# Kernel optimization log

Hardware: AMD Instinct MI355X
Metric: run time of the kernel (lower is better)

The kernel has to match this reference:

```python
import jax, jax.numpy as jnp
import numpy as np

H = 1024          # hidden_size
E = 2 * H         # expansion e
S_DIM = 128       # shared q/k dim s
B, S = 4, 2048


def setup_inputs() -> dict:
    key = jax.random.key(0)
    ks = jax.random.split(key, 6)
    inputs = jax.random.normal(ks[0], (B, S, H), dtype=jnp.float32)
    W_uv = jax.random.normal(ks[1], (H, 2 * E + S_DIM), dtype=jnp.float32) * (1.0 / np.sqrt(H))
    b_uv = jnp.zeros((2 * E + S_DIM,), dtype=jnp.float32)
    gamma = jax.random.normal(ks[2], (2, S_DIM), dtype=jnp.float32) * 0.02
    beta = jnp.zeros((2, S_DIM), dtype=jnp.float32)
    W_out = jax.random.normal(ks[3], (E, H), dtype=jnp.float32) * (1.0 / np.sqrt(E))
    b_out = jnp.zeros((H,), dtype=jnp.float32)
    return {"inputs": inputs, "W_uv": W_uv, "b_uv": b_uv,
            "gamma": gamma, "beta": beta, "W_out": W_out, "b_out": b_out}


def reference(inputs, W_uv, b_uv, gamma, beta, W_out, b_out):
    seq_len = inputs.shape[1]
    # uv projection + SiLU
    uvb = jax.nn.silu(jnp.einsum('bsh,hf->bsf', inputs, W_uv) + b_uv)
    u = uvb[..., :E]                       # [B,S,E]
    v = uvb[..., E:2 * E]                  # [B,S,E]
    base = uvb[..., 2 * E:]                # [B,S,s]
    # per-head affine: [B,S,1,s]*[2,s] + [2,s] -> [B,S,2,s]
    qk = base[..., None, :] * gamma + beta
    q, k = qk[..., 0, :], qk[..., 1, :]    # [B,S,s] each
    scores = jnp.einsum('bns,bms->bnm', q, k) / seq_len   # [B,S,S]
    sq = jnp.square(jax.nn.relu(scores))
    attn_v = jnp.einsum('bnm,bme->bne', sq, v)            # [B,S,E]
    return jnp.einsum('bne,eh->bnh', u * attn_v, W_out) + b_out
```

## Files before the change

### kernel.cpp

```cpp
#include <hip/hip_runtime.h>
#include <stdint.h>


#define H_DIM  1024
#define E_DIM  2048
#define SD     128
#define B_SZ   4
#define S_LEN  2048
#define M_TOT  (B_SZ * S_LEN)
#define F_DIM  (2 * E_DIM + SD)

typedef _Float16 f16;
typedef __attribute__((ext_vector_type(4))) _Float16 f16x4;
typedef __attribute__((ext_vector_type(8))) _Float16 f16x8;
typedef __attribute__((ext_vector_type(16))) float f32x16;

__device__ __forceinline__ float silu_f(float x) { return x / (1.f + __expf(-x)); }

__device__ __forceinline__ void gload16(const void* g, void* l) {
  __builtin_amdgcn_global_load_lds(
      (const __attribute__((address_space(1))) void*)(uintptr_t)g,
      (__attribute__((address_space(3))) void*)(uint32_t)(uintptr_t)l,
      16, 0, 0);
}

__global__ __launch_bounds__(256) void cast_f16_k(const float* __restrict__ src,
                                                  f16* __restrict__ dst, long n) {
  long i = ((long)blockIdx.x * 256 + threadIdx.x) * 4;
  if (i < n) {
    float4 v = *(const float4*)(src + i);
    f16x4 h; h[0] = (f16)v.x; h[1] = (f16)v.y; h[2] = (f16)v.z; h[3] = (f16)v.w;
    *(f16x4*)(dst + i) = h;
  }
}

__global__ __launch_bounds__(256) void transpose_cast_k(const float* __restrict__ src,
                                                        f16* __restrict__ dst, int R, int C) {
  __shared__ float tile[32][33];
  int c0 = blockIdx.x * 32, r0 = blockIdx.y * 32;
  int tx = threadIdx.x & 31, ty = threadIdx.x >> 5;
  for (int i = ty; i < 32; i += 8) tile[i][tx] = src[(long)(r0 + i) * C + c0 + tx];
  __syncthreads();
  for (int i = ty; i < 32; i += 8) dst[(long)(c0 + i) * R + r0 + tx] = (f16)tile[tx][i];
}

template <int MODE>
__global__ __launch_bounds__(512, 2) void gemm256(
    const f16* __restrict__ Ag, const f16* __restrict__ Bg,
    float* __restrict__ F0, f16* __restrict__ O0, f16* __restrict__ O1,
    const f16* __restrict__ I0, const float* __restrict__ C0)
{
  constexpr int K  = (MODE == 0) ? H_DIM : 2048;
  constexpr int NT = K / 64;

  __shared__ f16 As[2][256][64];
  __shared__ f16 Bs[2][256][64];

  const int t    = threadIdx.x;
  const int w    = t >> 6;
  const int lane = t & 63;
  const int lo5  = lane & 31;
  const int hi   = lane >> 5;
  const int wm   = w >> 2;
  const int wn   = w & 3;

  const int gx  = gridDim.x;
  const int nwg = gx * gridDim.y;
  const int lin = blockIdx.y * gx + blockIdx.x;
  const int cpx = nwg >> 3;
  const int wg  = (lin & 7) * cpx + (lin >> 3);
  const int n0  = (wg % gx) * 256;
  const int m0  = (wg / gx) * 256;
  const long z  = blockIdx.z;

  const f16* A = Ag + (MODE == 2 ? z * (long)S_LEN * S_LEN : 0);
  const f16* B = Bg + (MODE == 2 ? z * (long)E_DIM * S_LEN : 0);

  auto stageA = [&](int bb, int half, int kt2) {
    const f16* g0 = A + (long)(m0 + half * 128) * K + kt2 * 64;
    f16* lb = &As[bb][half * 128][0];
#pragma unroll
    for (int j = 0; j < 2; j++) {
      int grp = (j << 3) + w;
      int rl  = (grp << 3) + (lane >> 3);
      gload16(g0 + (long)rl * K + (((lane & 7) ^ (lane >> 3) ^ (grp & 1)) << 3),
              lb + (grp << 9));
    }
  };
  auto stageB = [&](int bb, int half, int kt2) {
    const f16* g0 = B + (long)(n0 + half * 128) * K + kt2 * 64;
    f16* lb = &Bs[bb][half * 128][0];
#pragma unroll
    for (int j = 0; j < 2; j++) {
      int grp = (j << 3) + w;
      int rl  = (grp << 3) + (lane >> 3);
      gload16(g0 + (long)rl * K + (((lane & 7) ^ (lane >> 3) ^ (grp & 1)) << 3),
              lb + (grp << 9));
    }
  };

  f32x16 acc[4][2] = {};
  f16x8 a0[2][4], a1[2][4], b0[4], b1[4];

  const int swz = (lo5 & 7) ^ ((lo5 >> 3) & 1);
  const int rA  = wm * 64 + lo5;
  const int rB  = wn * 32 + lo5;

  auto loadA0 = [&](int bb) {
#pragma unroll
    for (int k = 0; k < 4; k++) {
      const int pc = ((((k << 1) + hi) ^ swz) << 3);
      a0[0][k] = *(const f16x8*)&As[bb][rA][pc];
      a0[1][k] = *(const f16x8*)&As[bb][rA + 32][pc];
    }
  };
  auto loadA1 = [&](int bb) {
#pragma unroll
    for (int k = 0; k < 4; k++) {
      const int pc = ((((k << 1) + hi) ^ swz) << 3);
      a1[0][k] = *(const f16x8*)&As[bb][128 + rA][pc];
      a1[1][k] = *(const f16x8*)&As[bb][128 + rA + 32][pc];
    }
  };
  auto loadB0 = [&](int bb) {
#pragma unroll
    for (int k = 0; k < 4; k++) {
      const int pc = ((((k << 1) + hi) ^ swz) << 3);
      b0[k] = *(const f16x8*)&Bs[bb][rB][pc];
    }
  };
  auto loadB1 = [&](int bb) {
#pragma unroll
    for (int k = 0; k < 4; k++) {
      const int pc = ((((k << 1) + hi) ^ swz) << 3);
      b1[k] = *(const f16x8*)&Bs[bb][128 + rB][pc];
    }
  };

#define MMA(Q, AV, BV) do {                                                      \
    __builtin_amdgcn_s_setprio(1);                                               \
    _Pragma("unroll")                                                            \
    for (int k_ = 0; k_ < 4; k_++) {                                             \
      acc[Q][0] = __builtin_amdgcn_mfma_f32_32x32x16_f16(AV[0][k_], BV[k_],      \
                                                         acc[Q][0], 0, 0, 0);    \
      acc[Q][1] = __builtin_amdgcn_mfma_f32_32x32x16_f16(AV[1][k_], BV[k_],      \
                                                         acc[Q][1], 0, 0, 0);    \
    }                                                                            \
    __builtin_amdgcn_s_setprio(0);                                               \
  } while (0)

  stageA(0, 0, 0); stageA(0, 1, 0); stageB(0, 0, 0); stageB(0, 1, 0);
  stageA(1, 0, 1); stageA(1, 1, 1); stageB(1, 0, 1); stageB(1, 1, 1);
  asm volatile("s_waitcnt vmcnt(8)" ::: "memory");
  __builtin_amdgcn_s_barrier();
  loadA0(0); loadB0(0);

  for (int kt = 0; kt < NT; ++kt) {
    const int bf = kt & 1;
    const bool s2    = (kt + 2 < NT);
    const bool lastt = (kt + 1 == NT);

    loadA1(bf);
    __builtin_amdgcn_sched_barrier(0);
    MMA(0, a0, b0);
    __builtin_amdgcn_s_barrier();

    if (s2) { stageA(bf, 0, kt + 2); stageB(bf, 0, kt + 2); }
    loadB1(bf);
    __builtin_amdgcn_sched_barrier(0);
    MMA(2, a1, b0);
    __builtin_amdgcn_s_barrier();

    if (s2) stageA(bf, 1, kt + 2);
    MMA(1, a0, b1);
    __builtin_amdgcn_s_barrier();

    if (s2) stageB(bf, 1, kt + 2);
    if (s2) { asm volatile("s_waitcnt vmcnt(8)" ::: "memory"); }
    else    { asm volatile("s_waitcnt vmcnt(0)" ::: "memory"); }
    __builtin_amdgcn_s_barrier();
    if (!lastt) { loadA0(bf ^ 1); loadB0(bf ^ 1); }
    __builtin_amdgcn_sched_barrier(0);
    MMA(3, a1, b1);
  }
#undef MMA

#pragma unroll
  for (int q = 0; q < 4; q++) {
    const int ms = q >> 1;
    const int ns = q & 1;
#pragma unroll
    for (int im = 0; im < 2; im++) {
      const int gc    = n0 + ns * 128 + wn * 32 + lo5;
      const int rbase = m0 + ms * 128 + wm * 64 + im * 32 + (hi << 2);
      if (MODE == 0) {
        const float bias = C0[gc];
        if (n0 < E_DIM) {
#pragma unroll
          for (int g = 0; g < 4; g++)
#pragma unroll
            for (int rr = 0; rr < 4; rr++) {
              int gr = rbase + (g << 3) + rr;
              O0[(long)gr * E_DIM + gc] = (f16)silu_f(acc[q][im][g * 4 + rr] + bias);
            }
        } else {
#pragma unroll
          for (int g = 0; g < 4; g++) {
            int gr0 = rbase + (g << 3);
            int b   = gr0 >> 11;
            int s0  = gr0 & (S_LEN - 1);
            f16x4 pk;
#pragma unroll
            for (int rr = 0; rr < 4; rr++) pk[rr] = (f16)silu_f(acc[q][im][g * 4 + rr] + bias);
            *(f16x4*)&O1[((long)b * E_DIM + (gc - E_DIM)) * S_LEN + s0] = pk;
          }
        }
      } else if (MODE == 2) {
        const long rowoff = z * S_LEN;
#pragma unroll
        for (int g = 0; g < 4; g++)
#pragma unroll
          for (int rr = 0; rr < 4; rr++) {
            int gr = rbase + (g << 3) + rr;
            long idx = (rowoff + gr) * (long)E_DIM + gc;
            O0[idx] = (f16)((float)I0[idx] * acc[q][im][g * 4 + rr]);
          }
      } else {
        const float bias = C0[gc];
#pragma unroll
        for (int g = 0; g < 4; g++)
#pragma unroll
          for (int rr = 0; rr < 4; rr++) {
            int gr = rbase + (g << 3) + rr;
            F0[(long)gr * H_DIM + gc] = acc[q][im][g * 4 + rr] * (1.0f / 17179869184.0f) + bias;
          }
      }
    }
  }
}

template <int MODE>
__global__ __launch_bounds__(256) void mfma_gemm(
    const f16* __restrict__ Ag, const f16* __restrict__ Bg,
    float* __restrict__ F0, f16* __restrict__ H0, const f16* __restrict__ H1,
    f16* __restrict__ H2, f16* __restrict__ H3,
    const float* __restrict__ C0, const float* __restrict__ C1,
    const float* __restrict__ C2)
{
  constexpr int K   = (MODE == 1) ? SD : H_DIM;
  constexpr int LDA = K, LDB = K;

  __shared__ f16 As[2][128][32];
  __shared__ f16 Bs[2][128][32];

  const int t    = threadIdx.x;
  const int w    = t >> 6;
  const int lane = t & 63;
  const int lo5  = lane & 31;
  const int hi   = lane >> 5;
  const int wy   = w >> 1, wx = w & 1;
  const int m0   = blockIdx.y * 128;
  const int n0   = blockIdx.x * 128;
  const long z   = blockIdx.z;

  const f16* A = Ag + (MODE == 1 ? z * (long)S_LEN * SD : 0);
  const f16* B = Bg + (MODE == 1 ? z * (long)S_LEN * SD : 0);

  const int srow = lane >> 2;
  const int scol = (((lane & 3) ^ ((srow >> 1) & 3))) * 8;
  const int rsw  = (lo5 >> 1) & 3;

  f32x16 acc[2][2] = {};

  for (int k0 = 0; k0 < K; k0 += 64) {
#pragma unroll
    for (int h = 0; h < 2; h++)
#pragma unroll
      for (int g16 = 0; g16 < 2; g16++) {
        const int r = (w << 5) + (g16 << 4);
        gload16(A + (long)(m0 + r + srow) * LDA + k0 + (h << 5) + scol, &As[h][r][0]);
        gload16(B + (long)(n0 + r + srow) * LDB + k0 + (h << 5) + scol, &Bs[h][r][0]);
      }
    __syncthreads();

#pragma unroll
    for (int ks = 0; ks < 4; ks++) {
      const int h  = ks >> 1;
      const int cl = ((ks & 1) << 1) + hi;
      const int kc = (cl ^ rsw) << 3;
      f16x8 av[2], bv[2];
#pragma unroll
      for (int i = 0; i < 2; i++)
        av[i] = *(const f16x8*)&As[h][(wy << 6) + (i << 5) + lo5][kc];
#pragma unroll
      for (int j = 0; j < 2; j++)
        bv[j] = *(const f16x8*)&Bs[h][(wx << 6) + (j << 5) + lo5][kc];
#pragma unroll
      for (int i = 0; i < 2; i++)
#pragma unroll
        for (int j = 0; j < 2; j++)
          acc[i][j] = __builtin_amdgcn_mfma_f32_32x32x16_f16(av[i], bv[j], acc[i][j], 0, 0, 0);
    }
    __syncthreads();
  }

  const int rb0 = m0 + (wy << 6) + (hi << 2);
  const int cb0 = n0 + (wx << 6) + lo5;

  if (MODE == 4) {
#pragma unroll
    for (int i = 0; i < 2; i++)
#pragma unroll
      for (int j = 0; j < 2; j++) {
        int jj = cb0 + (j << 5);
        float bias = C0[jj];
        float g0 = C1[jj], g1 = C1[SD + jj];
        float be0 = C2[jj], be1 = C2[SD + jj];
#pragma unroll
        for (int g = 0; g < 4; g++)
#pragma unroll
          for (int rr = 0; rr < 4; rr++) {
            int gr = rb0 + (i << 5) + (g << 3) + rr;
            float s = silu_f(acc[i][j][g * 4 + rr] + bias);
            H2[(long)gr * SD + jj] = (f16)(s * g0 + be0);
            H3[(long)gr * SD + jj] = (f16)(s * g1 + be1);
          }
      }
  } else {
#pragma unroll
    for (int i = 0; i < 2; i++)
#pragma unroll
      for (int j = 0; j < 2; j++) {
        int gc = cb0 + (j << 5);
#pragma unroll
        for (int g = 0; g < 4; g++)
#pragma unroll
          for (int rr = 0; rr < 4; rr++) {
            int gr = rb0 + (i << 5) + (g << 3) + rr;
            float tv = fmaxf(acc[i][j][g * 4 + rr], 0.f) * 64.f;
            H0[z * (long)S_LEN * S_LEN + (long)gr * S_LEN + gc] = (f16)(tv * tv);
          }
      }
  }
}

extern "C" void kernel_launch(void* const* d_in, const int* in_sizes, int n_in,
                              void* d_out, int out_size, void* d_ws, size_t ws_size,
                              hipStream_t stream) {
  const float* X     = (const float*)d_in[0];
  const float* W_uv  = (const float*)d_in[1];
  const float* b_uv  = (const float*)d_in[2];
  const float* gamma = (const float*)d_in[3];
  const float* beta  = (const float*)d_in[4];
  const float* W_out = (const float*)d_in[5];
  const float* b_out = (const float*)d_in[6];
  float* out = (float*)d_out;

  char* wp = (char*)d_ws;
  f16* Xh   = (f16*)wp; wp += (long)M_TOT * H_DIM * 2;
  f16* Wuvt = (f16*)wp; wp += (long)F_DIM * H_DIM * 2;
  f16* Wt   = (f16*)wp; wp += (long)H_DIM * E_DIM * 2;
  f16* u    = (f16*)wp; wp += (long)M_TOT * E_DIM * 2;
  f16* vt   = (f16*)wp; wp += (long)M_TOT * E_DIM * 2;
  f16* qh   = (f16*)wp; wp += (long)M_TOT * SD * 2;
  f16* kh   = (f16*)wp; wp += (long)M_TOT * SD * 2;
  f16* sq   = (f16*)wp; wp += (long)B_SZ * S_LEN * S_LEN * 2;
  f16* p    = (f16*)wp; wp += (long)M_TOT * E_DIM * 2;

  cast_f16_k<<<(M_TOT * H_DIM) / (256 * 4), 256, 0, stream>>>(X, Xh, (long)M_TOT * H_DIM);
  transpose_cast_k<<<dim3(F_DIM / 32, H_DIM / 32), 256, 0, stream>>>(W_uv, Wuvt, H_DIM, F_DIM);
  transpose_cast_k<<<dim3(H_DIM / 32, E_DIM / 32), 256, 0, stream>>>(W_out, Wt, E_DIM, H_DIM);

  gemm256<0><<<dim3(2 * E_DIM / 256, M_TOT / 256, 1), 512, 0, stream>>>(
      Xh, Wuvt, nullptr, u, vt, nullptr, b_uv);

  mfma_gemm<4><<<dim3(1, M_TOT / 128, 1), 256, 0, stream>>>(
      Xh, Wuvt + (long)2 * E_DIM * H_DIM, nullptr, nullptr, nullptr, qh, kh,
      b_uv + 2 * E_DIM, gamma, beta);

  mfma_gemm<1><<<dim3(S_LEN / 128, S_LEN / 128, B_SZ), 256, 0, stream>>>(
      qh, kh, nullptr, sq, nullptr, nullptr, nullptr, nullptr, nullptr, nullptr);

  gemm256<2><<<dim3(E_DIM / 256, S_LEN / 256, B_SZ), 512, 0, stream>>>(
      sq, vt, nullptr, p, nullptr, u, nullptr);

  gemm256<3><<<dim3(H_DIM / 256, M_TOT / 256, 1), 512, 0, stream>>>(
      p, Wt, out, nullptr, nullptr, nullptr, b_out);
}
```

Measured before the change: 378.1 us.

## Restructure GEMM main loop into finer-grained LDS-load/MFMA interleaving stages

Splits the per-quadrant MFMA blocks into half-size groups and reorders the LDS register loads and global-to-LDS staging across four barrier-separated phases. The A and B fragments are now loaded at the start of each iteration instead of being prefetched from the next buffer at the end, and the sched_barrier fences are removed so the compiler can schedule freely. The aim is to balance LDS reads and MFMA work per phase and shorten register live ranges. It gives up the cross-iteration prefetch of fragments, which may expose LDS latency at the top of each iteration.

```diff
diff --git a/kernel.cpp b/kernel.cpp
--- a/kernel.cpp
+++ b/kernel.cpp
@@ -106,20 +106,18 @@
   const int rA  = wm * 64 + lo5;
   const int rB  = wn * 32 + lo5;
 
-  auto loadA0 = [&](int bb) {
+  auto loadA0h = [&](int bb, int im) {
 #pragma unroll
     for (int k = 0; k < 4; k++) {
       const int pc = ((((k << 1) + hi) ^ swz) << 3);
-      a0[0][k] = *(const f16x8*)&As[bb][rA][pc];
-      a0[1][k] = *(const f16x8*)&As[bb][rA + 32][pc];
-    }
-  };
-  auto loadA1 = [&](int bb) {
+      a0[im][k] = *(const f16x8*)&As[bb][rA + im * 32][pc];
+    }
+  };
+  auto loadA1h = [&](int bb, int im) {
 #pragma unroll
     for (int k = 0; k < 4; k++) {
       const int pc = ((((k << 1) + hi) ^ swz) << 3);
-      a1[0][k] = *(const f16x8*)&As[bb][128 + rA][pc];
-      a1[1][k] = *(const f16x8*)&As[bb][128 + rA + 32][pc];
+      a1[im][k] = *(const f16x8*)&As[bb][128 + rA + im * 32][pc];
     }
   };
   auto loadB0 = [&](int bb) {
@@ -137,53 +135,55 @@
     }
   };
 
-#define MMA(Q, AV, BV) do {                                                      \
-    __builtin_amdgcn_s_setprio(1);                                               \
+#define MMA4(Q, IM, AV, BV) do {                                                 \
     _Pragma("unroll")                                                            \
-    for (int k_ = 0; k_ < 4; k_++) {                                             \
-      acc[Q][0] = __builtin_amdgcn_mfma_f32_32x32x16_f16(AV[0][k_], BV[k_],      \
-                                                         acc[Q][0], 0, 0, 0);    \
-      acc[Q][1] = __builtin_amdgcn_mfma_f32_32x32x16_f16(AV[1][k_], BV[k_],      \
-                                                         acc[Q][1], 0, 0, 0);    \
-    }                                                                            \
-    __builtin_amdgcn_s_setprio(0);                                               \
+    for (int k_ = 0; k_ < 4; k_++)                                               \
+      acc[Q][IM] = __builtin_amdgcn_mfma_f32_32x32x16_f16(AV[k_], BV[k_],        \
+                                                          acc[Q][IM], 0, 0, 0);  \
   } while (0)
 
   stageA(0, 0, 0); stageA(0, 1, 0); stageB(0, 0, 0); stageB(0, 1, 0);
   stageA(1, 0, 1); stageA(1, 1, 1); stageB(1, 0, 1); stageB(1, 1, 1);
   asm volatile("s_waitcnt vmcnt(8)" ::: "memory");
   __builtin_amdgcn_s_barrier();
-  loadA0(0); loadB0(0);
 
   for (int kt = 0; kt < NT; ++kt) {
     const int bf = kt & 1;
-    const bool s2    = (kt + 2 < NT);
-    const bool lastt = (kt + 1 == NT);
-
-    loadA1(bf);
-    __builtin_amdgcn_sched_barrier(0);
-    MMA(0, a0, b0);
+    const bool s2 = (kt + 2 < NT);
+
+    loadA0h(bf, 0); loadB0(bf); loadA0h(bf, 1);
+    __builtin_amdgcn_s_setprio(1);
+    MMA4(0, 0, a0[0], b0);
+    __builtin_amdgcn_s_setprio(0);
     __builtin_amdgcn_s_barrier();
 
     if (s2) { stageA(bf, 0, kt + 2); stageB(bf, 0, kt + 2); }
     loadB1(bf);
-    __builtin_amdgcn_sched_barrier(0);
-    MMA(2, a1, b0);
+    __builtin_amdgcn_s_setprio(1);
+    MMA4(0, 1, a0[1], b0);
+    MMA4(1, 0, a0[0], b1);
+    __builtin_amdgcn_s_setprio(0);
     __builtin_amdgcn_s_barrier();
 
+    if (s2) stageB(bf, 1, kt + 2);
+    loadA1h(bf, 0); loadA1h(bf, 1);
+    __builtin_amdgcn_s_setprio(1);
+    MMA4(1, 1, a0[1], b1);
+    MMA4(2, 0, a1[0], b0);
+    __builtin_amdgcn_s_setprio(0);
+    __builtin_amdgcn_s_barrier();
+
     if (s2) stageA(bf, 1, kt + 2);
-    MMA(1, a0, b1);
-    __builtin_amdgcn_s_barrier();
-
-    if (s2) stageB(bf, 1, kt + 2);
+    __builtin_amdgcn_s_setprio(1);
+    MMA4(2, 1, a1[1], b0);
+    MMA4(3, 0, a1[0], b1);
+    MMA4(3, 1, a1[1], b1);
+    __builtin_amdgcn_s_setprio(0);
     if (s2) { asm volatile("s_waitcnt vmcnt(8)" ::: "memory"); }
     else    { asm volatile("s_waitcnt vmcnt(0)" ::: "memory"); }
     __builtin_amdgcn_s_barrier();
-    if (!lastt) { loadA0(bf ^ 1); loadB0(bf ^ 1); }
-    __builtin_amdgcn_sched_barrier(0);
-    MMA(3, a1, b1);
-  }
-#undef MMA
+  }
+#undef MMA4
 
 #pragma unroll
   for (int q = 0; q < 4; q++) {
```

New measurement: 371.1 us (median of 2 runs). No clear change (-1.9%).
